# Performance work log

Measured on AMD Instinct MI355X. Metric: run time of the kernel, lower is better.

## Reference

```python
import jax, jax.numpy as jnp
import numpy as np

C = 512        # in_ch = n_heads * d_embed
NH = 8         # heads
DH = C // NH   # head dim = 64
G = 32         # groups
EPS_GN = 1e-6
EPS_LN = 1e-5


def group_norm(x, gamma, beta):
    # x: (B, C, H, W)
    B, Cc, H, W = x.shape
    xg = x.reshape(B, G, Cc // G, H, W)
    mu = xg.mean(axis=(2, 3, 4), keepdims=True)
    var = xg.var(axis=(2, 3, 4), keepdims=True)
    xg = (xg - mu) * jax.lax.rsqrt(var + EPS_GN)
    x = xg.reshape(B, Cc, H, W)
    return x * gamma[None, :, None, None] + beta[None, :, None, None]


def layer_norm(x, gamma, beta):
    mu = x.mean(axis=-1, keepdims=True)
    var = x.var(axis=-1, keepdims=True)
    return (x - mu) * jax.lax.rsqrt(var + EPS_LN) * gamma + beta


def mhsa(x, w_qkv, w_out, b_out):
    # x: (B, S, C); w_qkv: (C, 3C); w_out: (C, C)
    B, S, Cc = x.shape
    qkv = x @ w_qkv                                   # (B, S, 3C)
    q, k, v = jnp.split(qkv, 3, axis=-1)
    q = q.reshape(B, S, NH, DH).transpose(0, 2, 1, 3)  # (B, H, S, D)
    k = k.reshape(B, S, NH, DH).transpose(0, 2, 1, 3)
    v = v.reshape(B, S, NH, DH).transpose(0, 2, 1, 3)
    scores = jnp.einsum('bhsd,bhtd->bhst', q, k) / jnp.sqrt(jnp.float32(DH))
    attn = jax.nn.softmax(scores, axis=-1)
    o = jnp.einsum('bhst,bhtd->bhsd', attn, v)         # (B, H, S, D)
    o = o.transpose(0, 2, 1, 3).reshape(B, S, Cc)
    return o @ w_out + b_out


def conv1x1(x, w, b):
    # x: (B, C, H, W); w: (Cout, Cin)
    return jnp.einsum('oc,bchw->bohw', w, x) + b[None, :, None, None]


def reference(x, gn_g, gn_b, w_cin, b_cin,
              ln1_g, ln1_b, qkv1, out1_w, out1_b,
              ln2_g, ln2_b, qkv2, out2_w, out2_b,
              ln3_g, ln3_b, g1_w, g1_b, g2_w, g2_b,
              w_cout, b_cout):
    residue_long = x
    h = group_norm(x, gn_g, gn_b)
    h = conv1x1(h, w_cin, b_cin)
    B, Cc, H, W = h.shape
    h = h.reshape(B, Cc, H * W).transpose(0, 2, 1)     # (B, S, C)

    r = h
    h = mhsa(layer_norm(h, ln1_g, ln1_b), qkv1, out1_w, out1_b) + r
    r = h
    h = mhsa(layer_norm(h, ln2_g, ln2_b), qkv2, out2_w, out2_b) + r
    r = h
    g = layer_norm(h, ln3_g, ln3_b) @ g1_w + g1_b      # (B, S, 8C)
    val, gate = jnp.split(g, 2, axis=-1)
    h = (val * jax.nn.gelu(gate, approximate=False)) @ g2_w + g2_b
    h = h + r

    h = h.transpose(0, 2, 1).reshape(B, Cc, H, W)
    return conv1x1(h, w_cout, b_cout) + residue_long


def setup_inputs() -> dict:
    key = jax.random.key(0)
    ks = jax.random.split(key, 16)
    s = lambda n: 1.0 / np.sqrt(n)
    return {
        'x': jax.random.normal(ks[0], (8, C, 32, 32), jnp.float32),
        'gn_g': jnp.ones((C,), jnp.float32),
        'gn_b': jnp.zeros((C,), jnp.float32),
        'w_cin': jax.random.normal(ks[1], (C, C), jnp.float32) * s(C),
        'b_cin': jnp.zeros((C,), jnp.float32),
        'ln1_g': jnp.ones((C,), jnp.float32),
        'ln1_b': jnp.zeros((C,), jnp.float32),
        'qkv1': jax.random.normal(ks[2], (C, 3 * C), jnp.float32) * s(C),
        'out1_w': jax.random.normal(ks[3], (C, C), jnp.float32) * s(C),
        'out1_b': jnp.zeros((C,), jnp.float32),
        'ln2_g': jnp.ones((C,), jnp.float32),
        'ln2_b': jnp.zeros((C,), jnp.float32),
        'qkv2': jax.random.normal(ks[4], (C, 3 * C), jnp.float32) * s(C),
        'out2_w': jax.random.normal(ks[5], (C, C), jnp.float32) * s(C),
        'out2_b': jnp.zeros((C,), jnp.float32),
        'ln3_g': jnp.ones((C,), jnp.float32),
        'ln3_b': jnp.zeros((C,), jnp.float32),
        'g1_w': jax.random.normal(ks[6], (C, 8 * C), jnp.float32) * s(C),
        'g1_b': jnp.zeros((8 * C,), jnp.float32),
        'g2_w': jax.random.normal(ks[7], (4 * C, C), jnp.float32) * s(4 * C),
        'g2_b': jnp.zeros((C,), jnp.float32),
        'w_cout': jax.random.normal(ks[8], (C, C), jnp.float32) * s(C),
        'b_cout': jnp.zeros((C,), jnp.float32),
    }
```

## Files before the change

### kernel.cpp

```cpp
#include <hip/hip_runtime.h>
#include <hip/hip_bf16.h>
#include <math.h>

typedef __hip_bfloat16 bf16;

typedef __bf16 bf16x8 __attribute__((ext_vector_type(8)));
typedef float f32x4 __attribute__((ext_vector_type(4)));
typedef short shortx8 __attribute__((ext_vector_type(8)));

__device__ __forceinline__ float b2f_us(unsigned short u) {
    unsigned int v = ((unsigned int)u) << 16;
    return __builtin_bit_cast(float, v);
}
__device__ __forceinline__ unsigned short f2b_us(float f) {
    return __builtin_bit_cast(unsigned short, __float2bfloat16(f));
}
__device__ __forceinline__ float4 ld4(const float* p) { return *(const float4*)p; }
__device__ __forceinline__ float4 ld4(const bf16* p) {
    ushort4 u = *(const ushort4*)p;
    return make_float4(b2f_us(u.x), b2f_us(u.y), b2f_us(u.z), b2f_us(u.w));
}
__device__ __forceinline__ bf16x8 ldfrag(const bf16* p) {
    return __builtin_bit_cast(bf16x8, *(const shortx8*)p);
}
__device__ __forceinline__ f32x4 mfma16(bf16x8 a, bf16x8 b, f32x4 c) {
    return __builtin_amdgcn_mfma_f32_16x16x32_bf16(a, b, c, 0, 0, 0);
}
__device__ __forceinline__ void gload16(const bf16* g, bf16* l) {
    __builtin_amdgcn_global_load_lds(
        (const __attribute__((address_space(1))) void*)g,
        (__attribute__((address_space(3))) void*)l, 16, 0, 0);
}

struct WJob { const float* src; bf16* dst; int R, C, tile0, trans; };
struct WJobs { WJob j[8]; };

__global__ __launch_bounds__(256) void wconv_all(WJobs jobs) {
    __shared__ float tl[32][33];
    int bid = blockIdx.x;
    int ji = 0;
#pragma unroll
    for (int i = 1; i < 8; ++i)
        if (bid >= jobs.j[i].tile0) ji = i;
    WJob jb = jobs.j[ji];
    int t = bid - jb.tile0;
    int tc = jb.C >> 5;
    int tr_ = t / tc, tcx = t - tr_ * tc;
    int r0 = tr_ * 32, c0 = tcx * 32;
    const int tx = threadIdx.x & 31, ty = threadIdx.x >> 5;
    if (jb.trans) {
#pragma unroll
        for (int i = 0; i < 4; ++i)
            tl[ty + i * 8][tx] = jb.src[(long)(r0 + ty + i * 8) * jb.C + c0 + tx];
        __syncthreads();
#pragma unroll
        for (int i = 0; i < 4; ++i)
            jb.dst[(long)(c0 + ty + i * 8) * jb.R + r0 + tx] =
                __float2bfloat16(tl[tx][ty + i * 8]);
    } else {
#pragma unroll
        for (int i = 0; i < 4; ++i) {
            long idx = (long)(r0 + ty + i * 8) * jb.C + c0 + tx;
            jb.dst[idx] = __float2bfloat16(jb.src[idx]);
        }
    }
}

__global__ __launch_bounds__(256) void gn_stats_k(const float* __restrict__ x,
                                                  float* __restrict__ stats) {
    int bg = blockIdx.x;
    long base = (long)bg * 16384;
    int tid = threadIdx.x;
    float s = 0.f, sq = 0.f;
    for (int it = 0; it < 16; ++it) {
        float4 v = *(const float4*)(x + base + (long)it * 1024 + tid * 4);
        s += v.x + v.y + v.z + v.w;
        sq += v.x * v.x + v.y * v.y + v.z * v.z + v.w * v.w;
    }
#pragma unroll
    for (int off = 32; off; off >>= 1) {
        s += __shfl_down(s, off);
        sq += __shfl_down(sq, off);
    }
    __shared__ float r0[4], r1[4];
    if ((tid & 63) == 0) { r0[tid >> 6] = s; r1[tid >> 6] = sq; }
    __syncthreads();
    if (tid == 0) {
        s = r0[0] + r0[1] + r0[2] + r0[3];
        sq = r1[0] + r1[1] + r1[2] + r1[3];
        float mu = s * (1.f / 16384.f);
        float var = sq * (1.f / 16384.f) - mu * mu;
        stats[bg] = mu;
        stats[256 + bg] = rsqrtf(var + 1e-6f);
    }
}

__global__ __launch_bounds__(256) void gnxt_k(const float* __restrict__ x,
                                              const float* __restrict__ stats,
                                              const float* __restrict__ gng,
                                              const float* __restrict__ gnb,
                                              bf16* __restrict__ xt) {
    const int b = blockIdx.z;
    const int c0 = blockIdx.y * 64, s0 = blockIdx.x * 64;
    __shared__ float t[64][65];
    const int tx = threadIdx.x & 15, ty = threadIdx.x >> 4;
#pragma unroll
    for (int i = 0; i < 4; ++i) {
        int c = c0 + ty + i * 16;
        float rs = stats[256 + b * 32 + (c >> 4)];
        float ga = gng[c] * rs;
        float be = gnb[c] - stats[b * 32 + (c >> 4)] * ga;
        float4 v = *(const float4*)(x + ((long)b * 512 + c) * 1024 + s0 + tx * 4);
        t[ty + i * 16][tx * 4 + 0] = v.x * ga + be;
        t[ty + i * 16][tx * 4 + 1] = v.y * ga + be;
        t[ty + i * 16][tx * 4 + 2] = v.z * ga + be;
        t[ty + i * 16][tx * 4 + 3] = v.w * ga + be;
    }
    __syncthreads();
#pragma unroll
    for (int i = 0; i < 4; ++i) {
        int s = s0 + ty + i * 16;
        ushort4 o;
        o.x = f2b_us(t[tx * 4 + 0][ty + i * 16]);
        o.y = f2b_us(t[tx * 4 + 1][ty + i * 16]);
        o.z = f2b_us(t[tx * 4 + 2][ty + i * 16]);
        o.w = f2b_us(t[tx * 4 + 3][ty + i * 16]);
        *(ushort4*)(xt + ((long)b * 1024 + s) * 512 + c0 + tx * 4) = o;
    }
}

__global__ __launch_bounds__(256) void ln_k(const bf16* __restrict__ in,
                                            const float* __restrict__ g,
                                            const float* __restrict__ bvec,
                                            bf16* __restrict__ out) {
    long row = blockIdx.x;
    const bf16* p = in + row * 512;
    int tid = threadIdx.x;
    float v0 = b2f_us(__builtin_bit_cast(unsigned short, p[tid]));
    float v1 = b2f_us(__builtin_bit_cast(unsigned short, p[tid + 256]));
    float s = v0 + v1, sq = v0 * v0 + v1 * v1;
#pragma unroll
    for (int off = 32; off; off >>= 1) {
        s += __shfl_down(s, off);
        sq += __shfl_down(sq, off);
    }
    __shared__ float r0[4], r1[4];
    if ((tid & 63) == 0) { r0[tid >> 6] = s; r1[tid >> 6] = sq; }
    __syncthreads();
    s = r0[0] + r0[1] + r0[2] + r0[3];
    sq = r1[0] + r1[1] + r1[2] + r1[3];
    float mu = s * (1.f / 512.f);
    float var = sq * (1.f / 512.f) - mu * mu;
    float rs = rsqrtf(var + 1e-5f);
    out[row * 512 + tid] = __float2bfloat16((v0 - mu) * rs * g[tid] + bvec[tid]);
    out[row * 512 + tid + 256] =
        __float2bfloat16((v1 - mu) * rs * g[tid + 256] + bvec[tid + 256]);
}

template <bool HASBIAS, bool HASRES, int BN, bool VSPLIT>
__global__ __launch_bounds__(256, 3) void mm_k(
    const bf16* __restrict__ A, const bf16* __restrict__ Bw,
    const float* __restrict__ bias, const bf16* __restrict__ res,
    bf16* __restrict__ C, bf16* __restrict__ vtout,
    int lda, int ldb, int ldc, int NT) {
    constexpr int NJ = BN / 64 * 2;
    __shared__ bf16 sA[8192];
    __shared__ bf16 sB[BN == 128 ? 8192 : 4096];
    const int lane = threadIdx.x & 63, wave = threadIdx.x >> 6;
    const int lr = lane & 15, lg = lane >> 4;
    const int wm = wave >> 1, wn = wave & 1;
    const int m0 = blockIdx.y * 128, n0 = blockIdx.x * BN;

    f32x4 acc[4][NJ];
#pragma unroll
    for (int i = 0; i < 4; ++i)
#pragma unroll
        for (int j = 0; j < NJ; ++j) acc[i][j] = (f32x4){0.f, 0.f, 0.f, 0.f};

    for (int t = 0; t < NT; ++t) {
        const int k0 = t * 64;
#pragma unroll
        for (int q = 0; q < 4; ++q) {
            int st = wave * 4 + q;
            int kh = st >> 3, sm = st & 7;
            gload16(A + (long)(m0 + sm * 16 + lr) * lda + k0 + kh * 32 + lg * 8,
                    &sA[st << 9]);
        }
        if (BN == 128) {
#pragma unroll
            for (int q = 0; q < 4; ++q) {
                int st = wave * 4 + q;
                int kh = st >> 3, sn = st & 7;
                gload16(Bw + (long)(n0 + sn * 16 + lr) * ldb + k0 + kh * 32 + lg * 8,
                        &sB[st << 9]);
            }
        } else {
#pragma unroll
            for (int q = 0; q < 2; ++q) {
                int bs = wave * 2 + q;
                int kh = bs >> 2, sn = bs & 3;
                gload16(Bw + (long)(n0 + sn * 16 + lr) * ldb + k0 + kh * 32 + lg * 8,
                        &sB[bs << 9]);
            }
        }
        asm volatile("s_waitcnt vmcnt(0) lgkmcnt(0)" ::: "memory");
        __builtin_amdgcn_s_barrier();
#pragma unroll
        for (int kh = 0; kh < 2; ++kh) {
            bf16x8 af[4], bfr[NJ];
#pragma unroll
            for (int i = 0; i < 4; ++i)
                af[i] = ldfrag(&sA[((kh * 8 + wm * 4 + i) << 9) + lane * 8]);
#pragma unroll
            for (int j = 0; j < NJ; ++j) {
                int bs = BN == 128 ? (kh * 8 + wn * 4 + j) : (kh * 4 + wn * 2 + j);
                bfr[j] = ldfrag(&sB[(bs << 9) + lane * 8]);
            }
#pragma unroll
            for (int i = 0; i < 4; ++i)
#pragma unroll
                for (int j = 0; j < NJ; ++j)
                    acc[i][j] = mfma16(af[i], bfr[j], acc[i][j]);
        }
        __builtin_amdgcn_s_barrier();
    }

    if (VSPLIT && n0 >= 1024) {
#pragma unroll
        for (int i = 0; i < 4; ++i) {
            int row = m0 + wm * 64 + i * 16 + lg * 4;
            int bb = row >> 10, ss = row & 1023;
#pragma unroll
            for (int j = 0; j < NJ; ++j) {
                int col = n0 + wn * (BN / 2) + j * 16 + lr;
                int v = col - 1024;
                int hh = v >> 6, dd = v & 63;
                ushort4 o4;
                o4.x = f2b_us(acc[i][j][0]);
                o4.y = f2b_us(acc[i][j][1]);
                o4.z = f2b_us(acc[i][j][2]);
                o4.w = f2b_us(acc[i][j][3]);
                *(ushort4*)(vtout + ((long)(bb * 8 + hh) * 64 + dd) * 1024 + ss) = o4;
            }
        }
        return;
    }
#pragma unroll
    for (int i = 0; i < 4; ++i) {
        int row = m0 + wm * 64 + i * 16 + lg * 4;
#pragma unroll
        for (int j = 0; j < NJ; ++j) {
            int col = n0 + wn * (BN / 2) + j * 16 + lr;
            float bv = HASBIAS ? bias[col] : 0.f;
#pragma unroll
            for (int r = 0; r < 4; ++r) {
                float v = acc[i][j][r] + bv;
                if (HASRES)
                    v += b2f_us(__builtin_bit_cast(unsigned short,
                             res[(long)(row + r) * ldc + col]));
                C[(long)(row + r) * ldc + col] = __float2bfloat16(v);
            }
        }
    }
}

__global__ __launch_bounds__(256, 2) void mm_geglu_k(
    const bf16* __restrict__ A, const bf16* __restrict__ Bv,
    const bf16* __restrict__ Bg, const float* __restrict__ bias,
    bf16* __restrict__ C, int NT) {
    __shared__ bf16 sA[8192];
    __shared__ bf16 sB[8192];
    const int lane = threadIdx.x & 63, wave = threadIdx.x >> 6;
    const int lr = lane & 15, lg = lane >> 4;
    const int wm = wave >> 1, wn = wave & 1;
    const int m0 = blockIdx.y * 128, n0 = blockIdx.x * 64;

    f32x4 accv[4][2], accg[4][2];
#pragma unroll
    for (int i = 0; i < 4; ++i)
#pragma unroll
        for (int j = 0; j < 2; ++j) {
            accv[i][j] = (f32x4){0.f, 0.f, 0.f, 0.f};
            accg[i][j] = (f32x4){0.f, 0.f, 0.f, 0.f};
        }

    for (int t = 0; t < NT; ++t) {
        const int k0 = t * 64;
#pragma unroll
        for (int q = 0; q < 4; ++q) {
            int st = wave * 4 + q;
            int kh = st >> 3, sm = st & 7;
            gload16(A + (long)(m0 + sm * 16 + lr) * 512 + k0 + kh * 32 + lg * 8,
                    &sA[st << 9]);
            const bf16* bsrc = (sm < 4) ? Bv : Bg;
            int sn = sm & 3;
            gload16(bsrc + (long)(n0 + sn * 16 + lr) * 512 + k0 + kh * 32 + lg * 8,
                    &sB[st << 9]);
        }
        asm volatile("s_waitcnt vmcnt(0) lgkmcnt(0)" ::: "memory");
        __builtin_amdgcn_s_barrier();
#pragma unroll
        for (int kh = 0; kh < 2; ++kh) {
            bf16x8 af[4], bv_[2], bg_[2];
#pragma unroll
            for (int i = 0; i < 4; ++i)
                af[i] = ldfrag(&sA[((kh * 8 + wm * 4 + i) << 9) + lane * 8]);
#pragma unroll
            for (int j = 0; j < 2; ++j) {
                bv_[j] = ldfrag(&sB[((kh * 8 + wn * 2 + j) << 9) + lane * 8]);
                bg_[j] = ldfrag(&sB[((kh * 8 + 4 + wn * 2 + j) << 9) + lane * 8]);
            }
#pragma unroll
            for (int i = 0; i < 4; ++i)
#pragma unroll
                for (int j = 0; j < 2; ++j) {
                    accv[i][j] = mfma16(af[i], bv_[j], accv[i][j]);
                    accg[i][j] = mfma16(af[i], bg_[j], accg[i][j]);
                }
        }
        __builtin_amdgcn_s_barrier();
    }

#pragma unroll
    for (int i = 0; i < 4; ++i) {
        int row = m0 + wm * 64 + i * 16 + lg * 4;
#pragma unroll
        for (int j = 0; j < 2; ++j) {
            int col = n0 + (wn * 2 + j) * 16 + lr;
            float bv = bias[col], bg2 = bias[2048 + col];
#pragma unroll
            for (int r = 0; r < 4; ++r) {
                float v = accv[i][j][r] + bv;
                float g = accg[i][j][r] + bg2;
                float gl = 0.5f * g * (1.f + erff(g * 0.70710678118654752f));
                C[(long)(row + r) * 2048 + col] = __float2bfloat16(v * gl);
            }
        }
    }
}

__global__ __launch_bounds__(256) void attn_mfma_k(const bf16* __restrict__ qkv,
                                                   const bf16* __restrict__ vt,
                                                   bf16* __restrict__ o) {
    const int wave = threadIdx.x >> 6, lane = threadIdx.x & 63;
    const int lr = lane & 15, lg = lane >> 4;
    const int h = blockIdx.y, b = blockIdx.z;
    const int q0 = blockIdx.x * 128 + wave * 32;
    __shared__ bf16 sKV[16384];
    __shared__ bf16 plds[4][16][72];
    bf16* pl = &plds[wave][0][0];
    const bf16* qbase = qkv + (long)b * 1024 * 1536 + h * 64;
    const bf16* kbase = qbase + 512;
    const bf16* vbase = vt + ((long)(b * 8 + h) * 64) * 1024;

    bf16x8 qf[2][2];
#pragma unroll
    for (int s = 0; s < 2; ++s) {
        const bf16* qp = qbase + (long)(q0 + s * 16 + lr) * 1536 + lg * 8;
#pragma unroll
        for (int c = 0; c < 2; ++c) {
            shortx8 raw = *(const shortx8*)(qp + c * 32);
            shortx8 sc;
#pragma unroll
            for (int j = 0; j < 8; ++j)
                sc[j] = __builtin_bit_cast(short,
                    f2b_us(b2f_us((unsigned short)raw[j]) * 0.125f));
            qf[s][c] = __builtin_bit_cast(bf16x8, sc);
        }
    }

    f32x4 of[2][4];
    float mrow[2][4], lrow[2][4];
#pragma unroll
    for (int s = 0; s < 2; ++s)
#pragma unroll
        for (int r = 0; r < 4; ++r) {
            of[s][r] = (f32x4){0.f, 0.f, 0.f, 0.f};
            mrow[s][r] = -1e30f;
            lrow[s][r] = 0.f;
        }

    auto computeKV = [&](const bf16* base) {
        f32x4 sf[2][4];
        __builtin_amdgcn_s_setprio(1);
#pragma unroll
        for (int kt = 0; kt < 4; ++kt) {
            bf16x8 k0f = ldfrag(base + (kt * 2) * 512 + lane * 8);
            bf16x8 k1f = ldfrag(base + (kt * 2 + 1) * 512 + lane * 8);
#pragma unroll
            for (int s = 0; s < 2; ++s) {
                f32x4 z = {0.f, 0.f, 0.f, 0.f};
                z = mfma16(qf[s][0], k0f, z);
                z = mfma16(qf[s][1], k1f, z);
                sf[s][kt] = z;
            }
        }
        __builtin_amdgcn_s_setprio(0);

        bf16x8 pa[2][2];
#pragma unroll
        for (int s = 0; s < 2; ++s) {
            float mt[4];
#pragma unroll
            for (int r = 0; r < 4; ++r)
                mt[r] = fmaxf(fmaxf(sf[s][0][r], sf[s][1][r]),
                              fmaxf(sf[s][2][r], sf[s][3][r]));
#pragma unroll
            for (int m = 1; m < 16; m <<= 1)
#pragma unroll
                for (int r = 0; r < 4; ++r)
                    mt[r] = fmaxf(mt[r], __shfl_xor(mt[r], m));
            float need = mt[0] - mrow[s][0];
#pragma unroll
            for (int r = 1; r < 4; ++r) need = fmaxf(need, mt[r] - mrow[s][r]);
            if (!__all(need <= 8.f)) {
#pragma unroll
                for (int r = 0; r < 4; ++r) {
                    float mn = fmaxf(mrow[s][r], mt[r]);
                    float al = __expf(mrow[s][r] - mn);
                    mrow[s][r] = mn;
                    lrow[s][r] *= al;
#pragma unroll
                    for (int dt = 0; dt < 4; ++dt) of[s][dt][r] *= al;
                }
            }
            float psum[4] = {0.f, 0.f, 0.f, 0.f};
#pragma unroll
            for (int kt = 0; kt < 4; ++kt)
#pragma unroll
                for (int r = 0; r < 4; ++r) {
                    float p = __expf(sf[s][kt][r] - mrow[s][r]);
                    psum[r] += p;
                    pl[(lg * 4 + r) * 72 + kt * 16 + lr] = __float2bfloat16(p);
                }
#pragma unroll
            for (int m = 1; m < 16; m <<= 1)
#pragma unroll
                for (int r = 0; r < 4; ++r)
                    psum[r] += __shfl_xor(psum[r], m);
#pragma unroll
            for (int r = 0; r < 4; ++r) lrow[s][r] += psum[r];
            pa[s][0] = ldfrag(pl + lr * 72 + lg * 8);
            pa[s][1] = ldfrag(pl + lr * 72 + 32 + lg * 8);
        }
        __builtin_amdgcn_s_setprio(1);
#pragma unroll
        for (int dt = 0; dt < 4; ++dt) {
            bf16x8 v0f = ldfrag(base + (8 + dt * 2) * 512 + lane * 8);
            bf16x8 v1f = ldfrag(base + (8 + dt * 2 + 1) * 512 + lane * 8);
#pragma unroll
            for (int s = 0; s < 2; ++s) {
                of[s][dt] = mfma16(pa[s][0], v0f, of[s][dt]);
                of[s][dt] = mfma16(pa[s][1], v1f, of[s][dt]);
            }
        }
        __builtin_amdgcn_s_setprio(0);
    };

    for (int t = 0; t < 8; ++t) {
        const int kv0 = t * 128;
#pragma unroll
        for (int q = 0; q < 8; ++q) {
            int st = wave * 8 + q;
            int chunk = st >> 4, r = st & 15;
            int kvb = kv0 + chunk * 64;
            const bf16* src;
            if (r < 8)
                src = kbase + (long)(kvb + (r >> 1) * 16 + lr) * 1536 +
                      (r & 1) * 32 + lg * 8;
            else {
                int vs = r - 8;
                src = vbase + (long)((vs >> 1) * 16 + lr) * 1024 + kvb +
                      (vs & 1) * 32 + lg * 8;
            }
            gload16(src, &sKV[st << 9]);
        }
        asm volatile("s_waitcnt vmcnt(0) lgkmcnt(0)" ::: "memory");
        __builtin_amdgcn_s_barrier();
        computeKV(&sKV[0]);
        computeKV(&sKV[8192]);
        __builtin_amdgcn_s_barrier();
    }

#pragma unroll
    for (int s = 0; s < 2; ++s) {
        bf16* op = o + ((long)b * 1024 + q0 + s * 16 + lg * 4) * 512 + h * 64 + lr;
#pragma unroll
        for (int r = 0; r < 4; ++r) {
            float inv = 1.f / lrow[s][r];
#pragma unroll
            for (int dt = 0; dt < 4; ++dt)
                op[(long)r * 512 + dt * 16] = __float2bfloat16(of[s][dt][r] * inv);
        }
    }
}

__global__ __launch_bounds__(256) void outepi_k(const bf16* __restrict__ tmp,
                                                const float* __restrict__ bcout,
                                                const float* __restrict__ x,
                                                float* __restrict__ out) {
    const int b = blockIdx.z;
    const int o0 = blockIdx.y * 64, s0 = blockIdx.x * 64;
    __shared__ float t[64][65];
    const int tx = threadIdx.x & 15, ty = threadIdx.x >> 4;
#pragma unroll
    for (int i = 0; i < 4; ++i) {
        int s = s0 + ty + i * 16;
        float4 v = ld4(tmp + ((long)b * 1024 + s) * 512 + o0 + tx * 4);
        t[ty + i * 16][tx * 4 + 0] = v.x;
        t[ty + i * 16][tx * 4 + 1] = v.y;
        t[ty + i * 16][tx * 4 + 2] = v.z;
        t[ty + i * 16][tx * 4 + 3] = v.w;
    }
    __syncthreads();
#pragma unroll
    for (int i = 0; i < 4; ++i) {
        int o = o0 + ty + i * 16;
        long idx = ((long)b * 512 + o) * 1024 + s0 + tx * 4;
        float4 xr = *(const float4*)(x + idx);
        float bc = bcout[o];
        float4 w;
        w.x = t[tx * 4 + 0][ty + i * 16] + bc + xr.x;
        w.y = t[tx * 4 + 1][ty + i * 16] + bc + xr.y;
        w.z = t[tx * 4 + 2][ty + i * 16] + bc + xr.z;
        w.w = t[tx * 4 + 3][ty + i * 16] + bc + xr.w;
        *(float4*)(out + idx) = w;
    }
}

extern "C" void kernel_launch(void* const* d_in, const int* in_sizes, int n_in,
                              void* d_out, int out_size, void* d_ws, size_t ws_size,
                              hipStream_t stream) {
    const float* x = (const float*)d_in[0];
    const float* gn_g = (const float*)d_in[1];
    const float* gn_b = (const float*)d_in[2];
    const float* w_cin = (const float*)d_in[3];
    const float* b_cin = (const float*)d_in[4];
    const float* ln1_g = (const float*)d_in[5];
    const float* ln1_b = (const float*)d_in[6];
    const float* qkv1w = (const float*)d_in[7];
    const float* out1_w = (const float*)d_in[8];
    const float* out1_b = (const float*)d_in[9];
    const float* ln2_g = (const float*)d_in[10];
    const float* ln2_b = (const float*)d_in[11];
    const float* qkv2w = (const float*)d_in[12];
    const float* out2_w = (const float*)d_in[13];
    const float* out2_b = (const float*)d_in[14];
    const float* ln3_g = (const float*)d_in[15];
    const float* ln3_b = (const float*)d_in[16];
    const float* g1_w = (const float*)d_in[17];
    const float* g1_b = (const float*)d_in[18];
    const float* g2_w = (const float*)d_in[19];
    const float* g2_b = (const float*)d_in[20];
    const float* w_cout = (const float*)d_in[21];
    const float* b_cout = (const float*)d_in[22];
    float* out = (float*)d_out;

    char* ws = (char*)d_ws;
    float* stats = (float*)ws;
    bf16* wq1 = (bf16*)(ws + 4096);
    bf16* wo1 = wq1 + 1536 * 512;
    bf16* wq2 = wo1 + 512 * 512;
    bf16* wo2 = wq2 + 1536 * 512;
    bf16* wg1 = wo2 + 512 * 512;
    bf16* wg2 = wg1 + 4096 * 512;
    bf16* wci = wg2 + 512 * 2048;
    bf16* wco = wci + 512 * 512;
    bf16* h = wco + 512 * 512;
    bf16* h2 = h + (size_t)8192 * 512;
    bf16* lnb = h2 + (size_t)8192 * 512;
    bf16* qkv = lnb + (size_t)8192 * 512;
    bf16* obuf = qkv + (size_t)8192 * 1536;
    bf16* gg = qkv;
    bf16* vt = obuf;

    WJobs jobs;
    jobs.j[0] = {qkv1w, wq1, 512, 1536, 0, 1};
    jobs.j[1] = {out1_w, wo1, 512, 512, 768, 1};
    jobs.j[2] = {qkv2w, wq2, 512, 1536, 1024, 1};
    jobs.j[3] = {out2_w, wo2, 512, 512, 1792, 1};
    jobs.j[4] = {g1_w, wg1, 512, 4096, 2048, 1};
    jobs.j[5] = {g2_w, wg2, 2048, 512, 4096, 1};
    jobs.j[6] = {w_cin, wci, 512, 512, 5120, 0};
    jobs.j[7] = {w_cout, wco, 512, 512, 5376, 0};
    wconv_all<<<5632, 256, 0, stream>>>(jobs);

    gn_stats_k<<<256, 256, 0, stream>>>(x, stats);
    gnxt_k<<<dim3(16, 8, 8), 256, 0, stream>>>(x, stats, gn_g, gn_b, lnb);
    mm_k<true, false, 64, false><<<dim3(8, 64), 256, 0, stream>>>(
        lnb, wci, b_cin, nullptr, h, nullptr, 512, 512, 512, 8);

    ln_k<<<8192, 256, 0, stream>>>(h, ln1_g, ln1_b, lnb);
    mm_k<false, false, 128, true><<<dim3(12, 64), 256, 0, stream>>>(
        lnb, wq1, nullptr, nullptr, qkv, vt, 512, 512, 1536, 8);
    attn_mfma_k<<<dim3(8, 8, 8), 256, 0, stream>>>(qkv, vt, lnb);
    mm_k<true, true, 64, false><<<dim3(8, 64), 256, 0, stream>>>(
        lnb, wo1, out1_b, h, h2, nullptr, 512, 512, 512, 8);

    ln_k<<<8192, 256, 0, stream>>>(h2, ln2_g, ln2_b, lnb);
    mm_k<false, false, 128, true><<<dim3(12, 64), 256, 0, stream>>>(
        lnb, wq2, nullptr, nullptr, qkv, vt, 512, 512, 1536, 8);
    attn_mfma_k<<<dim3(8, 8, 8), 256, 0, stream>>>(qkv, vt, lnb);
    mm_k<true, true, 64, false><<<dim3(8, 64), 256, 0, stream>>>(
        lnb, wo2, out2_b, h2, h, nullptr, 512, 512, 512, 8);

    ln_k<<<8192, 256, 0, stream>>>(h, ln3_g, ln3_b, lnb);
    mm_geglu_k<<<dim3(32, 64), 256, 0, stream>>>(
        lnb, wg1, wg1 + (size_t)2048 * 512, g1_b, gg, 8);
    mm_k<true, true, 64, false><<<dim3(8, 64), 256, 0, stream>>>(
        gg, wg2, g2_b, h, h2, nullptr, 2048, 2048, 512, 32);

    mm_k<false, false, 64, false><<<dim3(8, 64), 256, 0, stream>>>(
        h2, wco, nullptr, nullptr, lnb, nullptr, 512, 512, 512, 8);
    outepi_k<<<dim3(16, 8, 8), 256, 0, stream>>>(lnb, b_cout, x, out);
}
```

Measured before the change: 407.3 us.

## Use 256-row, 512-thread GEMM tiles for QKV and GEGLU projections

Adds an mm256_k kernel and an mm256_geglu_k kernel that use 512-thread blocks covering 256 rows of M, with 8 waves each computing a 64x64 (or 64x32 value+gate) subtile. The grid is reordered so that blockIdx.x walks M, which lets consecutive blocks share the same weight tile. The QKV projections and the GEGLU up-projection now use these kernels, while the other GEMMs keep the original 128-row mm_k. The aim is to halve the weight-tile reloads per output and improve L2 locality, at the cost of more LDS per block and fewer blocks in the grid.

Measured after the change: 401.4 us. No clear change (-1.5%).

```diff
diff --git a/kernel.cpp b/kernel.cpp
--- a/kernel.cpp
+++ b/kernel.cpp
@@ -157,69 +157,56 @@
         __float2bfloat16((v1 - mu) * rs * g[tid + 256] + bvec[tid + 256]);
 }
 
-template <bool HASBIAS, bool HASRES, int BN, bool VSPLIT>
-__global__ __launch_bounds__(256, 3) void mm_k(
+template <bool HASBIAS, bool HASRES, bool VSPLIT>
+__global__ __launch_bounds__(512, 4) void mm256_k(
     const bf16* __restrict__ A, const bf16* __restrict__ Bw,
     const float* __restrict__ bias, const bf16* __restrict__ res,
     bf16* __restrict__ C, bf16* __restrict__ vtout,
     int lda, int ldb, int ldc, int NT) {
-    constexpr int NJ = BN / 64 * 2;
-    __shared__ bf16 sA[8192];
-    __shared__ bf16 sB[BN == 128 ? 8192 : 4096];
+    __shared__ bf16 sA[16384];
+    __shared__ bf16 sB[8192];
     const int lane = threadIdx.x & 63, wave = threadIdx.x >> 6;
     const int lr = lane & 15, lg = lane >> 4;
     const int wm = wave >> 1, wn = wave & 1;
-    const int m0 = blockIdx.y * 128, n0 = blockIdx.x * BN;
-
-    f32x4 acc[4][NJ];
+    const int m0 = blockIdx.x * 256, n0 = blockIdx.y * 128;
+
+    f32x4 acc[4][4];
 #pragma unroll
     for (int i = 0; i < 4; ++i)
 #pragma unroll
-        for (int j = 0; j < NJ; ++j) acc[i][j] = (f32x4){0.f, 0.f, 0.f, 0.f};
+        for (int j = 0; j < 4; ++j) acc[i][j] = (f32x4){0.f, 0.f, 0.f, 0.f};
 
     for (int t = 0; t < NT; ++t) {
         const int k0 = t * 64;
 #pragma unroll
         for (int q = 0; q < 4; ++q) {
             int st = wave * 4 + q;
-            int kh = st >> 3, sm = st & 7;
+            int kh = st >> 4, sm = st & 15;
             gload16(A + (long)(m0 + sm * 16 + lr) * lda + k0 + kh * 32 + lg * 8,
                     &sA[st << 9]);
         }
-        if (BN == 128) {
-#pragma unroll
-            for (int q = 0; q < 4; ++q) {
-                int st = wave * 4 + q;
-                int kh = st >> 3, sn = st & 7;
-                gload16(Bw + (long)(n0 + sn * 16 + lr) * ldb + k0 + kh * 32 + lg * 8,
-                        &sB[st << 9]);
-            }
-        } else {
-#pragma unroll
-            for (int q = 0; q < 2; ++q) {
-                int bs = wave * 2 + q;
-                int kh = bs >> 2, sn = bs & 3;
-                gload16(Bw + (long)(n0 + sn * 16 + lr) * ldb + k0 + kh * 32 + lg * 8,
-                        &sB[bs << 9]);
-            }
+#pragma unroll
+        for (int q = 0; q < 2; ++q) {
+            int bs = wave * 2 + q;
+            int kh = bs >> 3, sn = bs & 7;
+            gload16(Bw + (long)(n0 + sn * 16 + lr) * ldb + k0 + kh * 32 + lg * 8,
+                    &sB[bs << 9]);
         }
         asm volatile("s_waitcnt vmcnt(0) lgkmcnt(0)" ::: "memory");
         __builtin_amdgcn_s_barrier();
 #pragma unroll
         for (int kh = 0; kh < 2; ++kh) {
-            bf16x8 af[4], bfr[NJ];
+            bf16x8 af[4], bfr[4];
 #pragma unroll
             for (int i = 0; i < 4; ++i)
-                af[i] = ldfrag(&sA[((kh * 8 + wm * 4 + i) << 9) + lane * 8]);
-#pragma unroll
-            for (int j = 0; j < NJ; ++j) {
-                int bs = BN == 128 ? (kh * 8 + wn * 4 + j) : (kh * 4 + wn * 2 + j);
-                bfr[j] = ldfrag(&sB[(bs << 9) + lane * 8]);
-            }
+                af[i] = ldfrag(&sA[((kh * 16 + wm * 4 + i) << 9) + lane * 8]);
+#pragma unroll
+            for (int j = 0; j < 4; ++j)
+                bfr[j] = ldfrag(&sB[((kh * 8 + wn * 4 + j) << 9) + lane * 8]);
 #pragma unroll
             for (int i = 0; i < 4; ++i)
 #pragma unroll
-                for (int j = 0; j < NJ; ++j)
+                for (int j = 0; j < 4; ++j)
                     acc[i][j] = mfma16(af[i], bfr[j], acc[i][j]);
         }
         __builtin_amdgcn_s_barrier();
@@ -231,8 +218,8 @@
             int row = m0 + wm * 64 + i * 16 + lg * 4;
             int bb = row >> 10, ss = row & 1023;
 #pragma unroll
-            for (int j = 0; j < NJ; ++j) {
-                int col = n0 + wn * (BN / 2) + j * 16 + lr;
+            for (int j = 0; j < 4; ++j) {
+                int col = n0 + wn * 64 + j * 16 + lr;
                 int v = col - 1024;
                 int hh = v >> 6, dd = v & 63;
                 ushort4 o4;
@@ -249,8 +236,8 @@
     for (int i = 0; i < 4; ++i) {
         int row = m0 + wm * 64 + i * 16 + lg * 4;
 #pragma unroll
-        for (int j = 0; j < NJ; ++j) {
-            int col = n0 + wn * (BN / 2) + j * 16 + lr;
+        for (int j = 0; j < 4; ++j) {
+            int col = n0 + wn * 64 + j * 16 + lr;
             float bv = HASBIAS ? bias[col] : 0.f;
 #pragma unroll
             for (int r = 0; r < 4; ++r) {
@@ -264,16 +251,16 @@
     }
 }
 
-__global__ __launch_bounds__(256, 2) void mm_geglu_k(
+__global__ __launch_bounds__(512, 4) void mm256_geglu_k(
     const bf16* __restrict__ A, const bf16* __restrict__ Bv,
     const bf16* __restrict__ Bg, const float* __restrict__ bias,
     bf16* __restrict__ C, int NT) {
-    __shared__ bf16 sA[8192];
+    __shared__ bf16 sA[16384];
     __shared__ bf16 sB[8192];
     const int lane = threadIdx.x & 63, wave = threadIdx.x >> 6;
     const int lr = lane & 15, lg = lane >> 4;
     const int wm = wave >> 1, wn = wave & 1;
-    const int m0 = blockIdx.y * 128, n0 = blockIdx.x * 64;
+    const int m0 = blockIdx.x * 256, n0 = blockIdx.y * 64;
 
     f32x4 accv[4][2], accg[4][2];
 #pragma unroll
@@ -289,13 +276,18 @@
 #pragma unroll
         for (int q = 0; q < 4; ++q) {
             int st = wave * 4 + q;
-            int kh = st >> 3, sm = st & 7;
+            int kh = st >> 4, sm = st & 15;
             gload16(A + (long)(m0 + sm * 16 + lr) * 512 + k0 + kh * 32 + lg * 8,
                     &sA[st << 9]);
-            const bf16* bsrc = (sm < 4) ? Bv : Bg;
-            int sn = sm & 3;
+        }
+#pragma unroll
+        for (int q = 0; q < 2; ++q) {
+            int f = wave * 2 + q;
+            int kh = f >> 3, r = f & 7;
+            const bf16* bsrc = (r < 4) ? Bv : Bg;
+            int sn = r & 3;
             gload16(bsrc + (long)(n0 + sn * 16 + lr) * 512 + k0 + kh * 32 + lg * 8,
-                    &sB[st << 9]);
+                    &sB[f << 9]);
         }
         asm volatile("s_waitcnt vmcnt(0) lgkmcnt(0)" ::: "memory");
         __builtin_amdgcn_s_barrier();
@@ -304,7 +296,7 @@
             bf16x8 af[4], bv_[2], bg_[2];
 #pragma unroll
             for (int i = 0; i < 4; ++i)
-                af[i] = ldfrag(&sA[((kh * 8 + wm * 4 + i) << 9) + lane * 8]);
+                af[i] = ldfrag(&sA[((kh * 16 + wm * 4 + i) << 9) + lane * 8]);
 #pragma unroll
             for (int j = 0; j < 2; ++j) {
                 bv_[j] = ldfrag(&sB[((kh * 8 + wn * 2 + j) << 9) + lane * 8]);
@@ -334,6 +326,92 @@
                 float g = accg[i][j][r] + bg2;
                 float gl = 0.5f * g * (1.f + erff(g * 0.70710678118654752f));
                 C[(long)(row + r) * 2048 + col] = __float2bfloat16(v * gl);
+            }
+        }
+    }
+}
+
+template <bool HASBIAS, bool HASRES, int BN>
+__global__ __launch_bounds__(256, 3) void mm_k(
+    const bf16* __restrict__ A, const bf16* __restrict__ Bw,
+    const float* __restrict__ bias, const bf16* __restrict__ res,
+    bf16* __restrict__ C, int lda, int ldb, int ldc, int NT) {
+    constexpr int NJ = BN / 64 * 2;
+    __shared__ bf16 sA[8192];
+    __shared__ bf16 sB[BN == 128 ? 8192 : 4096];
+    const int lane = threadIdx.x & 63, wave = threadIdx.x >> 6;
+    const int lr = lane & 15, lg = lane >> 4;
+    const int wm = wave >> 1, wn = wave & 1;
+    const int m0 = blockIdx.y * 128, n0 = blockIdx.x * BN;
+
+    f32x4 acc[4][NJ];
+#pragma unroll
+    for (int i = 0; i < 4; ++i)
+#pragma unroll
+        for (int j = 0; j < NJ; ++j) acc[i][j] = (f32x4){0.f, 0.f, 0.f, 0.f};
+
+    for (int t = 0; t < NT; ++t) {
+        const int k0 = t * 64;
+#pragma unroll
+        for (int q = 0; q < 4; ++q) {
+            int st = wave * 4 + q;
+            int kh = st >> 3, sm = st & 7;
+            gload16(A + (long)(m0 + sm * 16 + lr) * lda + k0 + kh * 32 + lg * 8,
+                    &sA[st << 9]);
+        }
+        if (BN == 128) {
+#pragma unroll
+            for (int q = 0; q < 4; ++q) {
+                int st = wave * 4 + q;
+                int kh = st >> 3, sn = st & 7;
+                gload16(Bw + (long)(n0 + sn * 16 + lr) * ldb + k0 + kh * 32 + lg * 8,
+                        &sB[st << 9]);
+            }
+        } else {
+#pragma unroll
+            for (int q = 0; q < 2; ++q) {
+                int bs = wave * 2 + q;
+                int kh = bs >> 2, sn = bs & 3;
+                gload16(Bw + (long)(n0 + sn * 16 + lr) * ldb + k0 + kh * 32 + lg * 8,
+                        &sB[bs << 9]);
+            }
+        }
+        asm volatile("s_waitcnt vmcnt(0) lgkmcnt(0)" ::: "memory");
+        __builtin_amdgcn_s_barrier();
+#pragma unroll
+        for (int kh = 0; kh < 2; ++kh) {
+            bf16x8 af[4], bfr[NJ];
+#pragma unroll
+            for (int i = 0; i < 4; ++i)
+                af[i] = ldfrag(&sA[((kh * 8 + wm * 4 + i) << 9) + lane * 8]);
+#pragma unroll
+            for (int j = 0; j < NJ; ++j) {
+                int bs = BN == 128 ? (kh * 8 + wn * 4 + j) : (kh * 4 + wn * 2 + j);
+                bfr[j] = ldfrag(&sB[(bs << 9) + lane * 8]);
+            }
+#pragma unroll
+            for (int i = 0; i < 4; ++i)
+#pragma unroll
+                for (int j = 0; j < NJ; ++j)
+                    acc[i][j] = mfma16(af[i], bfr[j], acc[i][j]);
+        }
+        __builtin_amdgcn_s_barrier();
+    }
+
+#pragma unroll
+    for (int i = 0; i < 4; ++i) {
+        int row = m0 + wm * 64 + i * 16 + lg * 4;
+#pragma unroll
+        for (int j = 0; j < NJ; ++j) {
+            int col = n0 + wn * (BN / 2) + j * 16 + lr;
+            float bv = HASBIAS ? bias[col] : 0.f;
+#pragma unroll
+            for (int r = 0; r < 4; ++r) {
+                float v = acc[i][j][r] + bv;
+                if (HASRES)
+                    v += b2f_us(__builtin_bit_cast(unsigned short,
+                             res[(long)(row + r) * ldc + col]));
+                C[(long)(row + r) * ldc + col] = __float2bfloat16(v);
             }
         }
     }
@@ -587,30 +665,30 @@
 
     gn_stats_k<<<256, 256, 0, stream>>>(x, stats);
     gnxt_k<<<dim3(16, 8, 8), 256, 0, stream>>>(x, stats, gn_g, gn_b, lnb);
-    mm_k<true, false, 64, false><<<dim3(8, 64), 256, 0, stream>>>(
-        lnb, wci, b_cin, nullptr, h, nullptr, 512, 512, 512, 8);
+    mm_k<true, false, 64><<<dim3(8, 64), 256, 0, stream>>>(
+        lnb, wci, b_cin, nullptr, h, 512, 512, 512, 8);
 
     ln_k<<<8192, 256, 0, stream>>>(h, ln1_g, ln1_b, lnb);
-    mm_k<false, false, 128, true><<<dim3(12, 64), 256, 0, stream>>>(
+    mm256_k<false, false, true><<<dim3(32, 12), 512, 0, stream>>>(
         lnb, wq1, nullptr, nullptr, qkv, vt, 512, 512, 1536, 8);
     attn_mfma_k<<<dim3(8, 8, 8), 256, 0, stream>>>(qkv, vt, lnb);
-    mm_k<true, true, 64, false><<<dim3(8, 64), 256, 0, stream>>>(
-        lnb, wo1, out1_b, h, h2, nullptr, 512, 512, 512, 8);
+    mm_k<true, true, 64><<<dim3(8, 64), 256, 0, stream>>>(
+        lnb, wo1, out1_b, h, h2, 512, 512, 512, 8);
 
     ln_k<<<8192, 256, 0, stream>>>(h2, ln2_g, ln2_b, lnb);
-    mm_k<false, false, 128, true><<<dim3(12, 64), 256, 0, stream>>>(
+    mm256_k<false, false, true><<<dim3(32, 12), 512, 0, stream>>>(
         lnb, wq2, nullptr, nullptr, qkv, vt, 512, 512, 1536, 8);
     attn_mfma_k<<<dim3(8, 8, 8), 256, 0, stream>>>(qkv, vt, lnb);
-    mm_k<true, true, 64, false><<<dim3(8, 64), 256, 0, stream>>>(
-        lnb, wo2, out2_b, h2, h, nullptr, 512, 512, 512, 8);
+    mm_k<true, true, 64><<<dim3(8, 64), 256, 0, stream>>>(
+        lnb, wo2, out2_b, h2, h, 512, 512, 512, 8);
 
     ln_k<<<8192, 256, 0, stream>>>(h, ln3_g, ln3_b, lnb);
-    mm_geglu_k<<<dim3(32, 64), 256, 0, stream>>>(
+    mm256_geglu_k<<<dim3(32, 32), 512, 0, stream>>>(
         lnb, wg1, wg1 + (size_t)2048 * 512, g1_b, gg, 8);
-    mm_k<true, true, 64, false><<<dim3(8, 64), 256, 0, stream>>>(
-        gg, wg2, g2_b, h, h2, nullptr, 2048, 2048, 512, 32);
-
-    mm_k<false, false, 64, false><<<dim3(8, 64), 256, 0, stream>>>(
-        h2, wco, nullptr, nullptr, lnb, nullptr, 512, 512, 512, 8);
+    mm_k<true, true, 64><<<dim3(8, 64), 256, 0, stream>>>(
+        gg, wg2, g2_b, h, h2, 2048, 2048, 512, 32);
+
+    mm_k<false, false, 64><<<dim3(8, 64), 256, 0, stream>>>(
+        h2, wco, nullptr, nullptr, lnb, 512, 512, 512, 8);
     outepi_k<<<dim3(16, 8, 8), 256, 0, stream>>>(lnb, b_cout, x, out);
 }
```
